# Kernel tuning notes

Measured on AMD Instinct MI355X. Metric: run time of the kernel, lower is better.

## Reference

```python
import jax, jax.numpy as jnp
import numpy as np

N_NODE, N_USER = 100000, 30000
N_REL, N_BASIS = 8, 30
EMB, OUT = 32, 32
E = 1600000
BATCH = 16384
H1, H2, H3 = 64, 32, 16
NEG_SLOPE = 0.2


def setup_inputs() -> dict:
    key = jax.random.key(0)
    ks = jax.random.split(key, 20)
    g = lambda k, shape: jax.random.normal(k, shape, dtype=jnp.float32) * 0.05
    inp = {
        "x_ids": jnp.arange(N_NODE, dtype=jnp.int64 if jax.config.jax_enable_x64 else jnp.int32),
        "edge_index": jax.random.randint(ks[0], (2, E), 0, N_NODE),
        "edge_type": jax.random.randint(ks[1], (E,), 0, N_REL),
        "users": jax.random.randint(ks[2], (BATCH,), 0, N_USER),
        "bundles": jax.random.randint(ks[3], (BATCH,), 0, N_NODE),
        # parameters
        "emb": g(ks[4], (N_NODE, EMB)),
        "basis": g(ks[5], (N_BASIS, EMB, OUT)),
        "weight": g(ks[6], (N_REL, N_BASIS)),
        "att": g(ks[7], (N_REL, 2 * OUT)),
        "root": g(ks[8], (EMB, OUT)),
        "bias": jnp.zeros((OUT,), jnp.float32),
        "W1": g(ks[9], (2 * OUT, H1)), "b1": jnp.zeros((H1,), jnp.float32),
        "W2": g(ks[10], (H1, H2)), "b2": jnp.zeros((H2,), jnp.float32),
        "W3": g(ks[11], (H2, H3)), "b3": jnp.zeros((H3,), jnp.float32),
        "Wo": g(ks[12], (H3, 1)), "bo": jnp.zeros((1,), jnp.float32),
    }
    return inp


def _tgcn_fwd(x_ids, edge_index, edge_type, users, bundles,
              emb, basis, weight, att, root, bias,
              W1, b1, W2, b2, W3, b3, Wo, bo):
    N = emb.shape[0]
    R = weight.shape[0]
    O = basis.shape[2]
    x = emb[x_ids]                                   # (N, F) embedding lookup
    # basis decomposition: (R, F, O)
    w = (weight @ basis.reshape(N_BASIS, -1)).reshape(R, EMB, O)
    # transform every node under every relation once, then gather per edge
    xh = jnp.einsum('nf,rfo->nro', x, w)             # (N, R, O)
    src, dst = edge_index[0], edge_index[1]          # j (source), i (target)
    h_i = xh[dst, edge_type]                         # (E, O)
    h_j = xh[src, edge_type]                         # (E, O)
    a = att[edge_type]                               # (E, 2O)
    alpha = (h_i * a[:, :O]).sum(-1) + (h_j * a[:, O:]).sum(-1)
    alpha = jax.nn.leaky_relu(alpha, NEG_SLOPE)
    # segment softmax keyed by (target node, relation)
    seg_key = dst * R + edge_type
    n_seg = N * R
    amax = jax.ops.segment_max(alpha, seg_key, num_segments=n_seg)
    ex = jnp.exp(alpha - amax[seg_key])
    denom = jax.ops.segment_sum(ex, seg_key, num_segments=n_seg)
    alpha = ex / (denom[seg_key] + 1e-16)
    # scatter-add weighted messages into target nodes
    agg = jax.ops.segment_sum(h_j * alpha[:, None], dst, num_segments=N)
    h = jax.nn.relu(agg + x @ root + bias)           # update + ReLU
    z = jnp.concatenate([h[users], h[bundles]], axis=1)  # (B, 2O)
    z = jax.nn.relu(z @ W1 + b1)
    z = jax.nn.relu(z @ W2 + b2)
    z = jax.nn.relu(z @ W3 + b3)
    return z @ Wo + bo                               # (B, 1) logits


def reference(x_ids, edge_index, edge_type, users, bundles,
              emb, basis, weight, att, root, bias,
              W1, b1, W2, b2, W3, b3, Wo, bo):
    return _tgcn_fwd(x_ids, edge_index, edge_type, users, bundles,
                     emb, basis, weight, att, root, bias,
                     W1, b1, W2, b2, W3, b3, Wo, bo)
```

## Files before the change

### kernel.cpp

```cpp
#include <hip/hip_runtime.h>
#include <hip/hip_bf16.h>

#define N_NODE 100000
#define N_REL  8
#define EMB    32
#define OUT    32
#define N_BASIS 30
#define E_EDGE 1600000
#define BATCH  16384
#define H1 64
#define H2 32
#define H3 16
#define NEG_SLOPE 0.2f

#define BSH   8
#define NBKT  391
#define BCAP  5120
#define PCH   2048
#define PARTB 782

#define K5T   64

#define NPB   32
#define NTILES (N_NODE / NPB)
#define K1GRID 782
#define XSS   36
#define RTS   36


struct SortSmem {
    unsigned ent[BCAP];
    unsigned ent2[BCAP];
    unsigned hist[256], dbase[256], dcur[256], sc[256];
};
struct K1Smem {
    float xs[2][NPB * XSS];
    float rootsT[OUT * RTS];
    float was[16 * RTS];
    float biass[OUT];
};
struct PartSmem {
    unsigned long long stage[PCH];
    unsigned hist[NBKT], lbase[NBKT], lcur[NBKT], gbase[NBKT];
    unsigned sc[256];
};

__device__ __forceinline__ void k0f_body(float* __restrict__ wl,
                                         const float* __restrict__ weight,
                                         const float* __restrict__ basis,
                                         const float* __restrict__ att,
                                         float* __restrict__ w,
                                         float* __restrict__ wa) {
    int t = threadIdx.x;
    for (int i = t; i < N_REL * EMB * OUT; i += 256) {
        int r = i >> 10, fo = i & 1023;
        float acc = 0.f;
        #pragma unroll
        for (int b = 0; b < N_BASIS; b++)
            acc = fmaf(weight[r * N_BASIS + b], basis[b * (EMB * OUT) + fo], acc);
        wl[i] = acc;
        w[i] = acc;
    }
    __syncthreads();
    for (int i = t; i < 512; i += 256) {
        int which = i >> 8, rf = i & 255, r = rf >> 5, f = rf & 31;
        const float* wrow = wl + (r * 32 + f) * 32;
        const float* arow = att + r * 64 + which * 32;
        float acc = 0.f;
        #pragma unroll
        for (int o = 0; o < 32; o++) acc = fmaf(wrow[o], arow[o], acc);
        wa[i] = acc;
    }
}

__device__ __forceinline__ void part_body(PartSmem& P, int bid,
                                          const int* __restrict__ src,
                                          const int* __restrict__ dst,
                                          const int* __restrict__ et,
                                          unsigned* __restrict__ bcnt,
                                          unsigned* __restrict__ part) {
    int t = threadIdx.x;
    for (int i = t; i < NBKT; i += 256) P.hist[i] = 0;
    __syncthreads();
    int beg = bid * PCH, end = min(beg + PCH, E_EDGE);
    int n = end - beg;
    int ng = n >> 2;
    int g0 = t, g1 = t + 256;
    bool has0 = g0 < ng, has1 = g1 < ng;
    int4 s0v = {}, d0v = {}, e0v = {}, s1v = {}, d1v = {}, e1v = {};
    if (has0) {
        s0v = *(const int4*)&src[beg + 4 * g0];
        d0v = *(const int4*)&dst[beg + 4 * g0];
        e0v = *(const int4*)&et[beg + 4 * g0];
    }
    if (has1) {
        s1v = *(const int4*)&src[beg + 4 * g1];
        d1v = *(const int4*)&dst[beg + 4 * g1];
        e1v = *(const int4*)&et[beg + 4 * g1];
    }
    if (has0) {
        atomicAdd(&P.hist[(unsigned)d0v.x >> BSH], 1u);
        atomicAdd(&P.hist[(unsigned)d0v.y >> BSH], 1u);
        atomicAdd(&P.hist[(unsigned)d0v.z >> BSH], 1u);
        atomicAdd(&P.hist[(unsigned)d0v.w >> BSH], 1u);
    }
    if (has1) {
        atomicAdd(&P.hist[(unsigned)d1v.x >> BSH], 1u);
        atomicAdd(&P.hist[(unsigned)d1v.y >> BSH], 1u);
        atomicAdd(&P.hist[(unsigned)d1v.z >> BSH], 1u);
        atomicAdd(&P.hist[(unsigned)d1v.w >> BSH], 1u);
    }
    __syncthreads();
    unsigned v0 = (2 * t < NBKT) ? P.hist[2 * t] : 0u;
    unsigned v1 = (2 * t + 1 < NBKT) ? P.hist[2 * t + 1] : 0u;
    unsigned s = v0 + v1;
    P.sc[t] = s;
    __syncthreads();
    for (int off = 1; off < 256; off <<= 1) {
        unsigned y = (t >= off) ? P.sc[t - off] : 0u;
        __syncthreads();
        P.sc[t] += y;
        __syncthreads();
    }
    unsigned ex = P.sc[t] - s;
    if (2 * t < NBKT)     { P.lbase[2 * t] = ex;          P.lcur[2 * t] = ex; }
    if (2 * t + 1 < NBKT) { P.lbase[2 * t + 1] = ex + v0; P.lcur[2 * t + 1] = ex + v0; }
    __syncthreads();
    #define K_PART_STAGE(dd, ss, ee) do {                                   \
        unsigned b_ = (unsigned)(dd) >> BSH;                                \
        unsigned ent_ = ((unsigned)((dd) & 255) << 20)                      \
                      | ((unsigned)(ss) << 3) | (unsigned)(ee);             \
        unsigned pos_ = atomicAdd(&P.lcur[b_], 1u);                         \
        P.stage[pos_] = ((unsigned long long)b_ << 32) | ent_; } while (0)
    if (has0) {
        K_PART_STAGE(d0v.x, s0v.x, e0v.x);
        K_PART_STAGE(d0v.y, s0v.y, e0v.y);
        K_PART_STAGE(d0v.z, s0v.z, e0v.z);
        K_PART_STAGE(d0v.w, s0v.w, e0v.w);
    }
    if (has1) {
        K_PART_STAGE(d1v.x, s1v.x, e1v.x);
        K_PART_STAGE(d1v.y, s1v.y, e1v.y);
        K_PART_STAGE(d1v.z, s1v.z, e1v.z);
        K_PART_STAGE(d1v.w, s1v.w, e1v.w);
    }
    #undef K_PART_STAGE
    __syncthreads();
    for (int i = t; i < NBKT; i += 256)
        if (P.hist[i]) P.gbase[i] = atomicAdd(&bcnt[i], P.hist[i]);
    __syncthreads();
    for (int i = t; i < n; i += 256) {
        unsigned long long s64 = P.stage[i];
        unsigned b = (unsigned)(s64 >> 32);
        unsigned ent = (unsigned)s64;
        part[b * BCAP + P.gbase[b] + (i - P.lbase[b])] = ent;
    }
}

__global__ __launch_bounds__(256) void k_pf(const int* __restrict__ src,
                                            const int* __restrict__ dst,
                                            const int* __restrict__ et,
                                            unsigned* __restrict__ bcnt,
                                            unsigned* __restrict__ part,
                                            const float* __restrict__ weight,
                                            const float* __restrict__ basis,
                                            const float* __restrict__ att,
                                            float* __restrict__ w,
                                            float* __restrict__ wa) {
    __shared__ union { PartSmem p; float wl[N_REL * EMB * OUT]; } u;
    if (blockIdx.x < PARTB)
        part_body(u.p, blockIdx.x, src, dst, et, bcnt, part);
    else
        k0f_body(u.wl, weight, basis, att, w, wa);
}

__device__ __forceinline__ void k1x_body(K1Smem& K, int bid0,
                                         const float* __restrict__ emb,
                                         const float* __restrict__ w,
                                         const float* __restrict__ wa,
                                         const float* __restrict__ root,
                                         const float* __restrict__ bias,
                                         unsigned short* __restrict__ xh,
                                         float* __restrict__ p_i,
                                         float* __restrict__ p_j,
                                         float* __restrict__ agg) {
    const int t = threadIdx.x;
    const int ro = t & 127;
    const int rhi = ro >> 5, olo = ro & 31;

    float wc0[EMB], wc1[EMB];
    #pragma unroll
    for (int f = 0; f < EMB; f++) {
        wc0[f] = w[rhi * 1024 + f * 32 + olo];
        wc1[f] = w[rhi * 1024 + 4096 + f * 32 + olo];
    }
    #pragma unroll
    for (int f = 0; f < EMB; f++) asm volatile("" : "+v"(wc0[f]), "+v"(wc1[f]));

    for (int i = t; i < EMB * OUT; i += 256) {
        int f = i >> 5, oo = i & 31;
        K.rootsT[oo * RTS + f] = root[i];
    }
    for (int i = t; i < 512; i += 256) {
        int which = i >> 8, r = (i >> 5) & 7, f = i & 31;
        K.was[(which * 8 + r) * RTS + f] = wa[i];
    }
    if (t < OUT) K.biass[t] = bias[t];

    const int sn = t >> 3, scn = t & 7;
    int tile = bid0;
    {
        float4 v = ((const float4*)(emb + (size_t)tile * NPB * EMB))[t];
        *(float4*)&K.xs[0][sn * XSS + scn * 4] = v;
    }
    __syncthreads();

    int buf = 0;
    for (; tile < NTILES; tile += K1GRID) {
        const int ntile = tile + K1GRID;
        const bool has = ntile < NTILES;
        float4 pf;
        if (has)
            pf = ((const float4*)(emb + (size_t)ntile * NPB * EMB))[t];

        const int n0 = tile * NPB;
        const float* xb = K.xs[buf];

        {
            const float4* xr = (const float4*)&xb[(t >> 3) * XSS];
            const float4* wi = (const float4*)&K.was[(t & 7) * RTS];
            const float4* wj = (const float4*)&K.was[(8 + (t & 7)) * RTS];
            float ai = 0.f, aj = 0.f;
            #pragma unroll
            for (int c = 0; c < 8; c++) {
                float4 xv = xr[c];
                float4 vi = wi[c], vj = wj[c];
                ai = fmaf(xv.x, vi.x, ai); ai = fmaf(xv.y, vi.y, ai);
                ai = fmaf(xv.z, vi.z, ai); ai = fmaf(xv.w, vi.w, ai);
                aj = fmaf(xv.x, vj.x, aj); aj = fmaf(xv.y, vj.y, aj);
                aj = fmaf(xv.z, vj.z, aj); aj = fmaf(xv.w, vj.w, aj);
            }
            p_i[n0 * N_REL + t] = ai;
            p_j[n0 * N_REL + t] = aj;
        }

        {
            const int o = t & 31, ng = t >> 5;
            const float4* rt = (const float4*)&K.rootsT[o * RTS];
            float4 r0 = rt[0], r1 = rt[1], r2 = rt[2], r3 = rt[3];
            float4 r4 = rt[4], r5 = rt[5], r6 = rt[6], r7 = rt[7];
            float bv = K.biass[o];
            #pragma unroll
            for (int q = 0; q < 4; q++) {
                int n = ng * 4 + q;
                const float4* xr = (const float4*)&xb[n * XSS];
                float g = bv;
                float4 xv;
                xv = xr[0]; g = fmaf(xv.x, r0.x, g); g = fmaf(xv.y, r0.y, g);
                            g = fmaf(xv.z, r0.z, g); g = fmaf(xv.w, r0.w, g);
                xv = xr[1]; g = fmaf(xv.x, r1.x, g); g = fmaf(xv.y, r1.y, g);
                            g = fmaf(xv.z, r1.z, g); g = fmaf(xv.w, r1.w, g);
                xv = xr[2]; g = fmaf(xv.x, r2.x, g); g = fmaf(xv.y, r2.y, g);
                            g = fmaf(xv.z, r2.z, g); g = fmaf(xv.w, r2.w, g);
                xv = xr[3]; g = fmaf(xv.x, r3.x, g); g = fmaf(xv.y, r3.y, g);
                            g = fmaf(xv.z, r3.z, g); g = fmaf(xv.w, r3.w, g);
                xv = xr[4]; g = fmaf(xv.x, r4.x, g); g = fmaf(xv.y, r4.y, g);
                            g = fmaf(xv.z, r4.z, g); g = fmaf(xv.w, r4.w, g);
                xv = xr[5]; g = fmaf(xv.x, r5.x, g); g = fmaf(xv.y, r5.y, g);
                            g = fmaf(xv.z, r5.z, g); g = fmaf(xv.w, r5.w, g);
                xv = xr[6]; g = fmaf(xv.x, r6.x, g); g = fmaf(xv.y, r6.y, g);
                            g = fmaf(xv.z, r6.z, g); g = fmaf(xv.w, r6.w, g);
                xv = xr[7]; g = fmaf(xv.x, r7.x, g); g = fmaf(xv.y, r7.y, g);
                            g = fmaf(xv.z, r7.z, g); g = fmaf(xv.w, r7.w, g);
                agg[(size_t)(n0 + n) * OUT + o] = g;
            }
        }

        {
            const int half = t >> 7;
            #pragma unroll 4
            for (int s = 0; s < 16; s++) {
                int n = 2 * s + half;
                const float4* xr = (const float4*)&xb[n * XSS];
                float a0 = 0.f, a1 = 0.f;
                #pragma unroll
                for (int c = 0; c < 8; c++) {
                    float4 xv = xr[c];
                    a0 = fmaf(xv.x, wc0[4 * c + 0], a0);
                    a0 = fmaf(xv.y, wc0[4 * c + 1], a0);
                    a0 = fmaf(xv.z, wc0[4 * c + 2], a0);
                    a0 = fmaf(xv.w, wc0[4 * c + 3], a0);
                    a1 = fmaf(xv.x, wc1[4 * c + 0], a1);
                    a1 = fmaf(xv.y, wc1[4 * c + 1], a1);
                    a1 = fmaf(xv.z, wc1[4 * c + 2], a1);
                    a1 = fmaf(xv.w, wc1[4 * c + 3], a1);
                }
                __hip_bfloat16 b0 = __float2bfloat16(a0);
                __hip_bfloat16 b1 = __float2bfloat16(a1);
                unsigned short* xp = xh + (size_t)(n0 + n) * 256;
                xp[ro]       = *(unsigned short*)&b0;
                xp[ro + 128] = *(unsigned short*)&b1;
            }
        }

        if (has)
            *(float4*)&K.xs[buf ^ 1][sn * XSS + scn * 4] = pf;
        __syncthreads();
        buf ^= 1;
    }
}

__device__ __forceinline__ void sort_body(SortSmem& S, int b,
                                          const unsigned* __restrict__ bcnt,
                                          const unsigned* __restrict__ part,
                                          int* __restrict__ payload,
                                          int* __restrict__ begp,
                                          int* __restrict__ endp) {
    int t = threadIdx.x;
    unsigned s0 = (unsigned)b * BCAP;
    int n = (int)bcnt[b];
    if (n > BCAP) n = BCAP;
    S.hist[t] = 0;
    __syncthreads();
    int n4 = n & ~3;
    for (int i = 4 * t; i < n4; i += 1024) {
        uint4 e4 = *(const uint4*)&part[s0 + i];
        S.ent[i + 0] = e4.x; atomicAdd(&S.hist[e4.x >> 20], 1u);
        S.ent[i + 1] = e4.y; atomicAdd(&S.hist[e4.y >> 20], 1u);
        S.ent[i + 2] = e4.z; atomicAdd(&S.hist[e4.z >> 20], 1u);
        S.ent[i + 3] = e4.w; atomicAdd(&S.hist[e4.w >> 20], 1u);
    }
    for (int i = n4 + t; i < n; i += 256) {
        unsigned e = part[s0 + i];
        S.ent[i] = e;
        atomicAdd(&S.hist[e >> 20], 1u);
    }
    __syncthreads();
    unsigned v = S.hist[t];
    S.sc[t] = v;
    __syncthreads();
    for (int off = 1; off < 256; off <<= 1) {
        unsigned y = (t >= off) ? S.sc[t - off] : 0u;
        __syncthreads();
        S.sc[t] += y;
        __syncthreads();
    }
    unsigned ex = S.sc[t] - v;
    S.dbase[t] = ex;
    S.dcur[t] = ex;
    __syncthreads();
    int d = (b << BSH) + t;
    if (d < N_NODE) {
        begp[d] = (int)(s0 + S.dbase[t]);
        endp[d] = (int)(s0 + S.dbase[t] + S.hist[t]);
    }
    for (int i = t; i < n; i += 256) {
        unsigned e = S.ent[i];
        unsigned pos = atomicAdd(&S.dcur[e >> 20], 1u);
        S.ent2[pos] = e;
    }
    __syncthreads();
    for (int i = 4 * t; i < n4; i += 1024) {
        uint4 o4 = { S.ent2[i + 0], S.ent2[i + 1], S.ent2[i + 2], S.ent2[i + 3] };
        *(uint4*)&payload[s0 + i] = o4;
    }
    for (int i = n4 + t; i < n; i += 256) payload[s0 + i] = (int)S.ent2[i];
}

__global__ __launch_bounds__(256) void k1x(const float* __restrict__ emb,
                                           const float* __restrict__ w,
                                           const float* __restrict__ wa,
                                           const float* __restrict__ root,
                                           const float* __restrict__ bias,
                                           unsigned short* __restrict__ xh,
                                           float* __restrict__ p_i,
                                           float* __restrict__ p_j,
                                           float* __restrict__ agg) {
    __shared__ K1Smem K;
    k1x_body(K, blockIdx.x, emb, w, wa, root, bias, xh, p_i, p_j, agg);
}

__global__ __launch_bounds__(256) void k_sort(const unsigned* __restrict__ bcnt,
                                              const unsigned* __restrict__ part,
                                              int* __restrict__ payload,
                                              int* __restrict__ begp,
                                              int* __restrict__ endp) {
    __shared__ SortSmem S;
    sort_body(S, blockIdx.x, bcnt, part, payload, begp, endp);
}

__global__ __launch_bounds__(256) void k_sx(const unsigned* __restrict__ bcnt,
                                            const unsigned* __restrict__ part,
                                            int* __restrict__ payload,
                                            int* __restrict__ begp,
                                            int* __restrict__ endp,
                                            const float* __restrict__ emb,
                                            const float* __restrict__ w,
                                            const float* __restrict__ wa,
                                            const float* __restrict__ root,
                                            const float* __restrict__ bias,
                                            unsigned short* __restrict__ xh,
                                            float* __restrict__ p_i,
                                            float* __restrict__ p_j,
                                            float* __restrict__ agg) {
    __shared__ union USmem { SortSmem s; K1Smem k; } u;
    if (blockIdx.x < K1GRID)
        k1x_body(u.k, blockIdx.x, emb, w, wa, root, bias, xh, p_i, p_j, agg);
    else
        sort_body(u.s, blockIdx.x - K1GRID, bcnt, part, payload, begp, endp);
}

__global__ __launch_bounds__(256) void k_agg(const int* __restrict__ begp,
                                             const int* __restrict__ endp,
                                             const int* __restrict__ payload,
                                             const float* __restrict__ p_i,
                                             const float* __restrict__ p_j,
                                             const unsigned short* __restrict__ xh,
                                             float* __restrict__ agg,
                                             int d0, int d1) {
    __shared__ float den[4][8];
    __shared__ float alw[4][64];
    const int wv = threadIdx.x >> 6;
    int d = d0 + blockIdx.x * 4 + wv;
    if (d >= d1) return;
    const int lane = threadIdx.x & 63;
    const int beg = begp[d], end = endp[d];
    const int cnt = end - beg;
    if (cnt == 0) return;

    float pid[8];
    #pragma unroll
    for (int k = 0; k < 8; k++) pid[k] = p_i[(d << 3) | k];

    if (cnt <= 64) {
        if (lane < 8) den[wv][lane] = 0.f;
        __threadfence_block();
        int sr = 0, r = 0; float ev = 0.f;
        if (lane < cnt) {
            sr = payload[beg + lane] & 0xFFFFF;
            r = sr & 7;
            float pi = pid[0];
            #pragma unroll
            for (int k = 1; k < 8; k++) pi = (r == k) ? pid[k] : pi;
            float a = pi + p_j[sr];
            a = (a >= 0.f) ? a : NEG_SLOPE * a;
            ev = __expf(a);
            atomicAdd(&den[wv][r], ev);
        }
        __threadfence_block();
        float de = den[wv][r];
        float al = ev / (de + 1e-16f);
        alw[wv][lane] = al;
        __threadfence_block();

        const int g16 = lane >> 4;
        const int o2 = (lane & 15) * 2;
        float a0 = 0.f, a1 = 0.f;
        for (int e0 = 0; e0 < cnt; e0 += 4) {
            int e = e0 + g16;
            bool ok = e < cnt;
            float alv = ok ? alw[wv][e] : 0.f;
            int idx = beg + (ok ? e : 0);
            unsigned sre = (unsigned)payload[idx] & 0xFFFFFu;
            unsigned dw = *(const unsigned*)&xh[(sre << 5) + o2];
            a0 = fmaf(alv, __uint_as_float((dw & 0xFFFFu) << 16), a0);
            a1 = fmaf(alv, __uint_as_float(dw & 0xFFFF0000u), a1);
        }
        a0 += __shfl_xor(a0, 16, 64); a0 += __shfl_xor(a0, 32, 64);
        a1 += __shfl_xor(a1, 16, 64); a1 += __shfl_xor(a1, 32, 64);
        if (lane < 16) {
            float2* ap = (float2*)&agg[(size_t)d * OUT + o2];
            float2 cur = *ap;
            cur.x += a0; cur.y += a1;
            *ap = cur;
        }
        return;
    }

    const int h = lane >> 5;
    const int o = lane & 31;
    float sex[8] = {0.f,0.f,0.f,0.f,0.f,0.f,0.f,0.f};
    for (int i = beg + lane; i < end; i += 64) {
        int sr = payload[i] & 0xFFFFF;
        int r = sr & 7;
        float pi = pid[0];
        #pragma unroll
        for (int k = 1; k < 8; k++) pi = (r == k) ? pid[k] : pi;
        float a = pi + p_j[sr];
        a = (a >= 0.f) ? a : NEG_SLOPE * a;
        float ev = __expf(a);
        #pragma unroll
        for (int k = 0; k < 8; k++) sex[k] += (r == k) ? ev : 0.f;
    }
    #pragma unroll
    for (int k = 0; k < 8; k++) {
        #pragma unroll
        for (int m = 1; m <= 32; m <<= 1) sex[k] += __shfl_xor(sex[k], m, 64);
    }
    float v0 = 0.f;
    for (int c = beg; c < end; c += 64) {
        int i = c + lane;
        int sr = 0; float al = 0.f;
        if (i < end) {
            sr = payload[i] & 0xFFFFF;
            int r = sr & 7;
            float pi = pid[0];
            #pragma unroll
            for (int k = 1; k < 8; k++) pi = (r == k) ? pid[k] : pi;
            float a = pi + p_j[sr];
            a = (a >= 0.f) ? a : NEG_SLOPE * a;
            float ev = __expf(a);
            float de = sex[0];
            #pragma unroll
            for (int k = 1; k < 8; k++) de = (r == k) ? sex[k] : de;
            al = ev / (de + 1e-16f);
        }
        int m = min(64, end - c);
        for (int j0 = 0; j0 < m; j0 += 2) {
            int e0 = j0 + h;
            float a0 = __shfl(al, e0, 64); int s0 = __shfl(sr, e0, 64);
            if (e0 < m) {
                float xv = __uint_as_float((unsigned)xh[((unsigned)s0 << 5) + o] << 16);
                v0 = fmaf(a0, xv, v0);
            }
        }
    }
    float vv = v0;
    vv += __shfl_xor(vv, 32, 64);
    if (h == 0) agg[(size_t)d * OUT + o] += vv;
}

__global__ __launch_bounds__(K5T, 1) void k5_mlp(const int* __restrict__ users,
                                                 const int* __restrict__ bundles,
                                                 const float* __restrict__ agg,
                                                 const float* __restrict__ W1,
                                                 const float* __restrict__ b1,
                                                 const float* __restrict__ W2,
                                                 const float* __restrict__ b2,
                                                 const float* __restrict__ W3,
                                                 const float* __restrict__ b3,
                                                 const float* __restrict__ Wo,
                                                 const float* __restrict__ bo,
                                                 float* __restrict__ out) {
    __shared__ float4 W1s[2 * OUT * H1 / 4];
    __shared__ float4 W2s[H1 * H2 / 4];
    __shared__ float4 W3s[H2 * H3 / 4];
    __shared__ float b1s[H1], b2s[H2], b3s[H3], Wos[H3];
    __shared__ float bos;
    __shared__ float zs[K5T * 65];
    __shared__ float h1s[K5T * 65];
    const int t = threadIdx.x;

    const float4* W14 = (const float4*)W1;
    const float4* W24 = (const float4*)W2;
    const float4* W34 = (const float4*)W3;
    for (int i = t; i < 1024; i += K5T) W1s[i] = W14[i];
    for (int i = t; i < 512; i += K5T) W2s[i] = W24[i];
    for (int i = t; i < 128; i += K5T) W3s[i] = W34[i];
    if (t < H2) b2s[t] = b2[t];
    if (t < H3) { b3s[t] = b3[t]; Wos[t] = Wo[t]; }
    if (t < H1) b1s[t] = b1[t];
    if (t == 0) bos = bo[0];

    const int item = blockIdx.x * K5T + t;
    const int u = users[item], v = bundles[item];
    const float4* av = (const float4*)agg;
    float* zrow = &zs[t * 65];
    float* h1row = &h1s[t * 65];

    #pragma unroll
    for (int c = 0; c < 8; c++) {
        float4 x = av[(size_t)u * 8 + c];
        zrow[4 * c + 0] = fmaxf(x.x, 0.f); zrow[4 * c + 1] = fmaxf(x.y, 0.f);
        zrow[4 * c + 2] = fmaxf(x.z, 0.f); zrow[4 * c + 3] = fmaxf(x.w, 0.f);
    }
    #pragma unroll
    for (int c = 0; c < 8; c++) {
        float4 x = av[(size_t)v * 8 + c];
        zrow[32 + 4 * c + 0] = fmaxf(x.x, 0.f); zrow[32 + 4 * c + 1] = fmaxf(x.y, 0.f);
        zrow[32 + 4 * c + 2] = fmaxf(x.z, 0.f); zrow[32 + 4 * c + 3] = fmaxf(x.w, 0.f);
    }
    __syncthreads();

    #pragma unroll 4
    for (int j4 = 0; j4 < 16; j4++) {
        float a0 = b1s[4 * j4 + 0], a1 = b1s[4 * j4 + 1];
        float a2 = b1s[4 * j4 + 2], a3 = b1s[4 * j4 + 3];
        #pragma unroll 16
        for (int k = 0; k < 2 * OUT; k++) {
            float zk = zrow[k];
            float4 wv = W1s[k * 16 + j4];
            a0 = fmaf(zk, wv.x, a0); a1 = fmaf(zk, wv.y, a1);
            a2 = fmaf(zk, wv.z, a2); a3 = fmaf(zk, wv.w, a3);
        }
        h1row[4 * j4 + 0] = fmaxf(a0, 0.f); h1row[4 * j4 + 1] = fmaxf(a1, 0.f);
        h1row[4 * j4 + 2] = fmaxf(a2, 0.f); h1row[4 * j4 + 3] = fmaxf(a3, 0.f);
    }

    #pragma unroll 4
    for (int j4 = 0; j4 < 8; j4++) {
        float a0 = b2s[4 * j4 + 0], a1 = b2s[4 * j4 + 1];
        float a2 = b2s[4 * j4 + 2], a3 = b2s[4 * j4 + 3];
        #pragma unroll 16
        for (int k = 0; k < H1; k++) {
            float hk = h1row[k];
            float4 wv = W2s[k * 8 + j4];
            a0 = fmaf(hk, wv.x, a0); a1 = fmaf(hk, wv.y, a1);
            a2 = fmaf(hk, wv.z, a2); a3 = fmaf(hk, wv.w, a3);
        }
        zrow[4 * j4 + 0] = fmaxf(a0, 0.f); zrow[4 * j4 + 1] = fmaxf(a1, 0.f);
        zrow[4 * j4 + 2] = fmaxf(a2, 0.f); zrow[4 * j4 + 3] = fmaxf(a3, 0.f);
    }

    float h3v[16];
    #pragma unroll
    for (int j4 = 0; j4 < 4; j4++) {
        float a0 = b3s[4 * j4 + 0], a1 = b3s[4 * j4 + 1];
        float a2 = b3s[4 * j4 + 2], a3 = b3s[4 * j4 + 3];
        #pragma unroll 16
        for (int k = 0; k < H2; k++) {
            float hk = zrow[k];
            float4 wv = W3s[k * 4 + j4];
            a0 = fmaf(hk, wv.x, a0); a1 = fmaf(hk, wv.y, a1);
            a2 = fmaf(hk, wv.z, a2); a3 = fmaf(hk, wv.w, a3);
        }
        h3v[4 * j4 + 0] = fmaxf(a0, 0.f); h3v[4 * j4 + 1] = fmaxf(a1, 0.f);
        h3v[4 * j4 + 2] = fmaxf(a2, 0.f); h3v[4 * j4 + 3] = fmaxf(a3, 0.f);
    }

    float acc = bos;
    #pragma unroll
    for (int k = 0; k < H3; k++) acc = fmaf(h3v[k], Wos[k], acc);
    out[item] = acc;
}

extern "C" void kernel_launch(void* const* d_in, const int* in_sizes, int n_in,
                              void* d_out, int out_size, void* d_ws, size_t ws_size,
                              hipStream_t stream) {
    (void)in_sizes; (void)n_in; (void)out_size;
    const int*   eidx   = (const int*)d_in[1];
    const int*   etype  = (const int*)d_in[2];
    const int*   users  = (const int*)d_in[3];
    const int*   bund   = (const int*)d_in[4];
    const float* emb    = (const float*)d_in[5];
    const float* basis  = (const float*)d_in[6];
    const float* weight = (const float*)d_in[7];
    const float* att    = (const float*)d_in[8];
    const float* root   = (const float*)d_in[9];
    const float* bias   = (const float*)d_in[10];
    const float* W1 = (const float*)d_in[11]; const float* b1 = (const float*)d_in[12];
    const float* W2 = (const float*)d_in[13]; const float* b2 = (const float*)d_in[14];
    const float* W3 = (const float*)d_in[15]; const float* b3 = (const float*)d_in[16];
    const float* Wo = (const float*)d_in[17]; const float* bo = (const float*)d_in[18];
    float* out = (float*)d_out;

    const int* src = eidx;
    const int* dst = eidx + E_EDGE;

    float* ws       = (float*)d_ws;
    float* w        = ws;
    float* wa       = w + N_REL * EMB * OUT;
    unsigned short* xh = (unsigned short*)(wa + 512);
    float* p_i      = (float*)(xh + (size_t)N_NODE * 256);
    float* p_j      = p_i + N_NODE * N_REL;
    float* agg      = p_j + N_NODE * N_REL;
    int*   payload  = (int*)(agg + (size_t)N_NODE * OUT);
    int*   begp     = payload + (size_t)NBKT * BCAP;
    int*   endp     = begp + N_NODE;
    unsigned* bcnt  = (unsigned*)(endp + N_NODE);
    unsigned* part_sep = bcnt + 512;
    size_t needed_mid = (size_t)((char*)(part_sep + (size_t)NBKT * BCAP) - (char*)d_ws);

    const bool mid = ws_size >= needed_mid;
    unsigned* part = mid ? part_sep : (unsigned*)agg;

    hipMemsetAsync(bcnt, 0, NBKT * sizeof(unsigned), stream);
    k_pf<<<PARTB + 1, 256, 0, stream>>>(src, dst, etype, bcnt, part,
                                        weight, basis, att, w, wa);
    if (mid) {
        k_sx<<<K1GRID + NBKT, 256, 0, stream>>>(bcnt, part, payload, begp, endp,
                                                emb, w, wa, root, bias,
                                                xh, p_i, p_j, agg);
    } else {
        k_sort<<<NBKT, 256, 0, stream>>>(bcnt, part, payload, begp, endp);
        k1x<<<K1GRID, 256, 0, stream>>>(emb, w, wa, root, bias, xh, p_i, p_j, agg);
    }
    k_agg<<<N_NODE / 4, 256, 0, stream>>>(begp, endp, payload, p_i, p_j, xh, agg,
                                          0, N_NODE);
    k5_mlp<<<BATCH / K5T, K5T, 0, stream>>>(users, bund, agg, W1, b1, W2, b2, W3, b3,
                                            Wo, bo, out);
}
```

Baseline: 304.5 us.

## Fuse node transform with edge partition; recompute basis weights per block

Each node-transform block now computes the basis-decomposed relation weights and the attention projections itself in shared memory, so the separate weight-producing block and its global round trip go away. The node transform then runs in the same launch as edge partitioning, with even and odd blocks interleaved, and sorting moves to its own launch afterwards. The aim is to overlap the compute-heavy transform with the memory-bound partition. In exchange, every one of the 782 transform blocks redoes the 8x1024x30 weight reduction, and the sort no longer overlaps with the transform.

New measurement: 398.8 us. +30.9%, slower.

```diff
diff --git a/kernel.cpp b/kernel.cpp
--- a/kernel.cpp
+++ b/kernel.cpp
@@ -33,45 +33,21 @@
     unsigned ent2[BCAP];
     unsigned hist[256], dbase[256], dcur[256], sc[256];
 };
-struct K1Smem {
+struct K1SmemB {
     float xs[2][NPB * XSS];
     float rootsT[OUT * RTS];
     float was[16 * RTS];
     float biass[OUT];
+};
+union K1U {
+    float wl[N_REL * EMB * OUT];
+    K1SmemB b;
 };
 struct PartSmem {
     unsigned long long stage[PCH];
     unsigned hist[NBKT], lbase[NBKT], lcur[NBKT], gbase[NBKT];
     unsigned sc[256];
 };
-
-__device__ __forceinline__ void k0f_body(float* __restrict__ wl,
-                                         const float* __restrict__ weight,
-                                         const float* __restrict__ basis,
-                                         const float* __restrict__ att,
-                                         float* __restrict__ w,
-                                         float* __restrict__ wa) {
-    int t = threadIdx.x;
-    for (int i = t; i < N_REL * EMB * OUT; i += 256) {
-        int r = i >> 10, fo = i & 1023;
-        float acc = 0.f;
-        #pragma unroll
-        for (int b = 0; b < N_BASIS; b++)
-            acc = fmaf(weight[r * N_BASIS + b], basis[b * (EMB * OUT) + fo], acc);
-        wl[i] = acc;
-        w[i] = acc;
-    }
-    __syncthreads();
-    for (int i = t; i < 512; i += 256) {
-        int which = i >> 8, rf = i & 255, r = rf >> 5, f = rf & 31;
-        const float* wrow = wl + (r * 32 + f) * 32;
-        const float* arow = att + r * 64 + which * 32;
-        float acc = 0.f;
-        #pragma unroll
-        for (int o = 0; o < 32; o++) acc = fmaf(wrow[o], arow[o], acc);
-        wa[i] = acc;
-    }
-}
 
 __device__ __forceinline__ void part_body(PartSmem& P, int bid,
                                           const int* __restrict__ src,
@@ -157,61 +133,75 @@
     }
 }
 
-__global__ __launch_bounds__(256) void k_pf(const int* __restrict__ src,
-                                            const int* __restrict__ dst,
-                                            const int* __restrict__ et,
-                                            unsigned* __restrict__ bcnt,
-                                            unsigned* __restrict__ part,
-                                            const float* __restrict__ weight,
-                                            const float* __restrict__ basis,
-                                            const float* __restrict__ att,
-                                            float* __restrict__ w,
-                                            float* __restrict__ wa) {
-    __shared__ union { PartSmem p; float wl[N_REL * EMB * OUT]; } u;
-    if (blockIdx.x < PARTB)
-        part_body(u.p, blockIdx.x, src, dst, et, bcnt, part);
-    else
-        k0f_body(u.wl, weight, basis, att, w, wa);
-}
-
-__device__ __forceinline__ void k1x_body(K1Smem& K, int bid0,
-                                         const float* __restrict__ emb,
-                                         const float* __restrict__ w,
-                                         const float* __restrict__ wa,
-                                         const float* __restrict__ root,
-                                         const float* __restrict__ bias,
-                                         unsigned short* __restrict__ xh,
-                                         float* __restrict__ p_i,
-                                         float* __restrict__ p_j,
-                                         float* __restrict__ agg) {
+__device__ __forceinline__ void k1xs_body(K1U& U, int bid0,
+                                          const float* __restrict__ emb,
+                                          const float* __restrict__ weight,
+                                          const float* __restrict__ basis,
+                                          const float* __restrict__ att,
+                                          const float* __restrict__ root,
+                                          const float* __restrict__ bias,
+                                          unsigned short* __restrict__ xh,
+                                          float* __restrict__ p_i,
+                                          float* __restrict__ p_j,
+                                          float* __restrict__ agg) {
     const int t = threadIdx.x;
     const int ro = t & 127;
     const int rhi = ro >> 5, olo = ro & 31;
 
+    for (int i = t; i < N_REL * EMB * OUT; i += 256) {
+        int r = i >> 10, fo = i & 1023;
+        float acc = 0.f;
+        #pragma unroll
+        for (int b = 0; b < N_BASIS; b++)
+            acc = fmaf(weight[r * N_BASIS + b], basis[b * (EMB * OUT) + fo], acc);
+        U.wl[i] = acc;
+    }
+    __syncthreads();
+
     float wc0[EMB], wc1[EMB];
     #pragma unroll
     for (int f = 0; f < EMB; f++) {
-        wc0[f] = w[rhi * 1024 + f * 32 + olo];
-        wc1[f] = w[rhi * 1024 + 4096 + f * 32 + olo];
+        wc0[f] = U.wl[rhi * 1024 + f * 32 + olo];
+        wc1[f] = U.wl[rhi * 1024 + 4096 + f * 32 + olo];
     }
     #pragma unroll
     for (int f = 0; f < EMB; f++) asm volatile("" : "+v"(wc0[f]), "+v"(wc1[f]));
 
-    for (int i = t; i < EMB * OUT; i += 256) {
-        int f = i >> 5, oo = i & 31;
-        K.rootsT[oo * RTS + f] = root[i];
-    }
-    for (int i = t; i < 512; i += 256) {
-        int which = i >> 8, r = (i >> 5) & 7, f = i & 31;
-        K.was[(which * 8 + r) * RTS + f] = wa[i];
-    }
-    if (t < OUT) K.biass[t] = bias[t];
+    float wav0, wav1;
+    {
+        int rf = t & 255, r = rf >> 5, f = rf & 31;
+        const float* wrow = &U.wl[(r * 32 + f) * 32];
+        const float* a0row = att + r * 64;
+        const float* a1row = att + r * 64 + 32;
+        float s0 = 0.f, s1 = 0.f;
+        #pragma unroll
+        for (int o = 0; o < 32; o++) {
+            s0 = fmaf(wrow[o], a0row[o], s0);
+            s1 = fmaf(wrow[o], a1row[o], s1);
+        }
+        wav0 = s0; wav1 = s1;
+    }
+    float rv0 = root[t], rv1 = root[t + 256];
+    float rv2 = root[t + 512], rv3 = root[t + 768];
+    float bv = (t < OUT) ? bias[t] : 0.f;
+    __syncthreads();
+
+    {
+        int rf = t & 255, r = rf >> 5, f = rf & 31;
+        U.b.was[r * RTS + f] = wav0;
+        U.b.was[(8 + r) * RTS + f] = wav1;
+    }
+    U.b.rootsT[(t & 31) * RTS + (t >> 5)] = rv0;
+    U.b.rootsT[((t + 256) & 31) * RTS + ((t + 256) >> 5)] = rv1;
+    U.b.rootsT[((t + 512) & 31) * RTS + ((t + 512) >> 5)] = rv2;
+    U.b.rootsT[((t + 768) & 31) * RTS + ((t + 768) >> 5)] = rv3;
+    if (t < OUT) U.b.biass[t] = bv;
 
     const int sn = t >> 3, scn = t & 7;
     int tile = bid0;
     {
         float4 v = ((const float4*)(emb + (size_t)tile * NPB * EMB))[t];
-        *(float4*)&K.xs[0][sn * XSS + scn * 4] = v;
+        *(float4*)&U.b.xs[0][sn * XSS + scn * 4] = v;
     }
     __syncthreads();
 
@@ -224,12 +214,12 @@
             pf = ((const float4*)(emb + (size_t)ntile * NPB * EMB))[t];
 
         const int n0 = tile * NPB;
-        const float* xb = K.xs[buf];
+        const float* xb = U.b.xs[buf];
 
         {
             const float4* xr = (const float4*)&xb[(t >> 3) * XSS];
-            const float4* wi = (const float4*)&K.was[(t & 7) * RTS];
-            const float4* wj = (const float4*)&K.was[(8 + (t & 7)) * RTS];
+            const float4* wi = (const float4*)&U.b.was[(t & 7) * RTS];
+            const float4* wj = (const float4*)&U.b.was[(8 + (t & 7)) * RTS];
             float ai = 0.f, aj = 0.f;
             #pragma unroll
             for (int c = 0; c < 8; c++) {
@@ -246,15 +236,15 @@
 
         {
             const int o = t & 31, ng = t >> 5;
-            const float4* rt = (const float4*)&K.rootsT[o * RTS];
+            const float4* rt = (const float4*)&U.b.rootsT[o * RTS];
             float4 r0 = rt[0], r1 = rt[1], r2 = rt[2], r3 = rt[3];
             float4 r4 = rt[4], r5 = rt[5], r6 = rt[6], r7 = rt[7];
-            float bv = K.biass[o];
+            float bvv = U.b.biass[o];
             #pragma unroll
             for (int q = 0; q < 4; q++) {
                 int n = ng * 4 + q;
                 const float4* xr = (const float4*)&xb[n * XSS];
-                float g = bv;
+                float g = bvv;
                 float4 xv;
                 xv = xr[0]; g = fmaf(xv.x, r0.x, g); g = fmaf(xv.y, r0.y, g);
                             g = fmaf(xv.z, r0.z, g); g = fmaf(xv.w, r0.w, g);
@@ -304,19 +294,67 @@
         }
 
         if (has)
-            *(float4*)&K.xs[buf ^ 1][sn * XSS + scn * 4] = pf;
+            *(float4*)&U.b.xs[buf ^ 1][sn * XSS + scn * 4] = pf;
         __syncthreads();
         buf ^= 1;
     }
 }
 
-__device__ __forceinline__ void sort_body(SortSmem& S, int b,
-                                          const unsigned* __restrict__ bcnt,
-                                          const unsigned* __restrict__ part,
-                                          int* __restrict__ payload,
-                                          int* __restrict__ begp,
-                                          int* __restrict__ endp) {
+__global__ __launch_bounds__(256) void k_px(const int* __restrict__ src,
+                                            const int* __restrict__ dst,
+                                            const int* __restrict__ et,
+                                            unsigned* __restrict__ bcnt,
+                                            unsigned* __restrict__ part,
+                                            const float* __restrict__ emb,
+                                            const float* __restrict__ weight,
+                                            const float* __restrict__ basis,
+                                            const float* __restrict__ att,
+                                            const float* __restrict__ root,
+                                            const float* __restrict__ bias,
+                                            unsigned short* __restrict__ xh,
+                                            float* __restrict__ p_i,
+                                            float* __restrict__ p_j,
+                                            float* __restrict__ agg) {
+    __shared__ union { PartSmem p; K1U k; } u;
+    if (blockIdx.x & 1)
+        part_body(u.p, blockIdx.x >> 1, src, dst, et, bcnt, part);
+    else
+        k1xs_body(u.k, blockIdx.x >> 1, emb, weight, basis, att, root, bias,
+                  xh, p_i, p_j, agg);
+}
+
+__global__ __launch_bounds__(256) void k_partk(const int* __restrict__ src,
+                                               const int* __restrict__ dst,
+                                               const int* __restrict__ et,
+                                               unsigned* __restrict__ bcnt,
+                                               unsigned* __restrict__ part) {
+    __shared__ PartSmem P;
+    part_body(P, blockIdx.x, src, dst, et, bcnt, part);
+}
+
+__global__ __launch_bounds__(256) void k1xs(const float* __restrict__ emb,
+                                            const float* __restrict__ weight,
+                                            const float* __restrict__ basis,
+                                            const float* __restrict__ att,
+                                            const float* __restrict__ root,
+                                            const float* __restrict__ bias,
+                                            unsigned short* __restrict__ xh,
+                                            float* __restrict__ p_i,
+                                            float* __restrict__ p_j,
+                                            float* __restrict__ agg) {
+    __shared__ K1U U;
+    k1xs_body(U, blockIdx.x, emb, weight, basis, att, root, bias,
+              xh, p_i, p_j, agg);
+}
+
+__global__ __launch_bounds__(256) void k_sort(const unsigned* __restrict__ bcnt,
+                                              const unsigned* __restrict__ part,
+                                              int* __restrict__ payload,
+                                              int* __restrict__ begp,
+                                              int* __restrict__ endp) {
+    __shared__ SortSmem S;
     int t = threadIdx.x;
+    int b = blockIdx.x;
     unsigned s0 = (unsigned)b * BCAP;
     int n = (int)bcnt[b];
     if (n > BCAP) n = BCAP;
@@ -365,49 +403,6 @@
         *(uint4*)&payload[s0 + i] = o4;
     }
     for (int i = n4 + t; i < n; i += 256) payload[s0 + i] = (int)S.ent2[i];
-}
-
-__global__ __launch_bounds__(256) void k1x(const float* __restrict__ emb,
-                                           const float* __restrict__ w,
-                                           const float* __restrict__ wa,
-                                           const float* __restrict__ root,
-                                           const float* __restrict__ bias,
-                                           unsigned short* __restrict__ xh,
-                                           float* __restrict__ p_i,
-                                           float* __restrict__ p_j,
-                                           float* __restrict__ agg) {
-    __shared__ K1Smem K;
-    k1x_body(K, blockIdx.x, emb, w, wa, root, bias, xh, p_i, p_j, agg);
-}
-
-__global__ __launch_bounds__(256) void k_sort(const unsigned* __restrict__ bcnt,
-                                              const unsigned* __restrict__ part,
-                                              int* __restrict__ payload,
-                                              int* __restrict__ begp,
-                                              int* __restrict__ endp) {
-    __shared__ SortSmem S;
-    sort_body(S, blockIdx.x, bcnt, part, payload, begp, endp);
-}
-
-__global__ __launch_bounds__(256) void k_sx(const unsigned* __restrict__ bcnt,
-                                            const unsigned* __restrict__ part,
-                                            int* __restrict__ payload,
-                                            int* __restrict__ begp,
-                                            int* __restrict__ endp,
-                                            const float* __restrict__ emb,
-                                            const float* __restrict__ w,
-                                            const float* __restrict__ wa,
-                                            const float* __restrict__ root,
-                                            const float* __restrict__ bias,
-                                            unsigned short* __restrict__ xh,
-                                            float* __restrict__ p_i,
-                                            float* __restrict__ p_j,
-                                            float* __restrict__ agg) {
-    __shared__ union USmem { SortSmem s; K1Smem k; } u;
-    if (blockIdx.x < K1GRID)
-        k1x_body(u.k, blockIdx.x, emb, w, wa, root, bias, xh, p_i, p_j, agg);
-    else
-        sort_body(u.s, blockIdx.x - K1GRID, bcnt, part, payload, begp, endp);
 }
 
 __global__ __launch_bounds__(256) void k_agg(const int* __restrict__ begp,
@@ -675,15 +670,16 @@
     unsigned* part = mid ? part_sep : (unsigned*)agg;
 
     hipMemsetAsync(bcnt, 0, NBKT * sizeof(unsigned), stream);
-    k_pf<<<PARTB + 1, 256, 0, stream>>>(src, dst, etype, bcnt, part,
-                                        weight, basis, att, w, wa);
     if (mid) {
-        k_sx<<<K1GRID + NBKT, 256, 0, stream>>>(bcnt, part, payload, begp, endp,
-                                                emb, w, wa, root, bias,
-                                                xh, p_i, p_j, agg);
+        k_px<<<2 * PARTB, 256, 0, stream>>>(src, dst, etype, bcnt, part,
+                                            emb, weight, basis, att, root, bias,
+                                            xh, p_i, p_j, agg);
+        k_sort<<<NBKT, 256, 0, stream>>>(bcnt, part, payload, begp, endp);
     } else {
+        k_partk<<<PARTB, 256, 0, stream>>>(src, dst, etype, bcnt, part);
         k_sort<<<NBKT, 256, 0, stream>>>(bcnt, part, payload, begp, endp);
-        k1x<<<K1GRID, 256, 0, stream>>>(emb, w, wa, root, bias, xh, p_i, p_j, agg);
+        k1xs<<<K1GRID, 256, 0, stream>>>(emb, weight, basis, att, root, bias,
+                                         xh, p_i, p_j, agg);
     }
     k_agg<<<N_NODE / 4, 256, 0, stream>>>(begp, endp, payload, p_i, p_j, xh, agg,
                                           0, N_NODE);
```
